# Optimization experiments

Hardware: AMD Instinct MI355X
Metric: run time of the kernel (lower is better)

The kernel has to match this reference:

```python
import jax, jax.numpy as jnp
import numpy as np

NUM_REGIONS = 32   # region labels are 1..NUM_REGIONS, 0 = background
EPS = 1e-8


def setup_inputs() -> dict:
    key = jax.random.key(0)
    k1, k2 = jax.random.split(key)
    B, D, H, W = 4, 160, 192, 192
    x = jax.random.normal(k1, (B, 1, D, H, W), dtype=jnp.float32)
    # precomputed connected-component label map (0 = background)
    region_map = jax.random.randint(k2, (B, D, H, W), 0, NUM_REGIONS + 1, dtype=jnp.int32)
    return {"x": x, "region_map": region_map}


def _per_volume_sums(xf, seg):
    # xf: [V] sigmoid probs, seg: [V] region ids in [0, NUM_REGIONS]
    xs = jax.ops.segment_sum(xf, seg, num_segments=NUM_REGIONS + 1)
    cnt = jax.ops.segment_sum(jnp.ones_like(xf), seg, num_segments=NUM_REGIONS + 1)
    return xs, cnt


def reference(x, region_map):
    B = x.shape[0]
    probs = jax.nn.sigmoid(x)                      # x.dim()==5 -> sigmoid
    xf = probs.reshape(B, -1)                      # [B, V]
    seg = region_map.reshape(B, -1)                # [B, V]
    xs, cnt = jax.vmap(_per_volume_sums)(xf, seg)  # [B, R+1] each
    xs_r = xs[:, 1:]                               # per-region sum of sigmoid(x)
    cnt_r = cnt[:, 1:]                             # per-region voxel count (= sum of binary y)
    # dice over the region: y==1 inside the region, so intersection == xs_r
    dice = 2.0 * xs_r / (xs_r + cnt_r + EPS)       # [B, R]
    valid = cnt_r > 0                              # region actually present
    n_valid = jnp.sum(valid, axis=-1)              # [B]
    mean_dice = jnp.sum(jnp.where(valid, dice, 0.0), axis=-1) / jnp.maximum(n_valid, 1)
    loss_b = jnp.where(n_valid > 0, 1.0 - mean_dice, 1.0)  # num_features==0 -> loss 1.0
    return jnp.mean(loss_b)
```

## Files before the change

kernel.cpp:

```cpp
#include <hip/hip_runtime.h>

#define NUM_REGIONS 32
#define NBINS 33
#define BATCH 4
#define DHW (160*192*192)
#define NVEC_PER_BATCH (DHW/4)
#define BLOCKS_PER_BATCH 512
#define NBLOCKS (BATCH*BLOCKS_PER_BATCH)
#define VEC_PER_BLOCK (NVEC_PER_BATCH/BLOCKS_PER_BATCH)
#define LDS_STRIDE 257
#define EPS 1e-8f

__global__ __launch_bounds__(256) void region_sums_kernel(
    const float* __restrict__ x,
    const int*   __restrict__ seg,
    float*       __restrict__ ws)
{
    __shared__ float hist[NBINS * LDS_STRIDE];
    const int tid = threadIdx.x;

    for (int i = tid; i < NBINS * LDS_STRIDE; i += 256) hist[i] = 0.0f;
    __syncthreads();

    const int  batch = blockIdx.x >> 9;
    const int  local = blockIdx.x & 511;
    const long vbase = (long)batch * NVEC_PER_BATCH + (long)local * VEC_PER_BLOCK;

    const float4* __restrict__ xv4 = (const float4*)x;
    const int4*   __restrict__ sv4 = (const int4*)seg;

    int    v  = tid;
    float4 xv = xv4[vbase + v];
    int4   sv = sv4[vbase + v];

    while (true) {
        int vn = v + 256;
        float4 xvn; int4 svn;
        bool more = (vn < VEC_PER_BLOCK);
        if (more) { xvn = xv4[vbase + vn]; svn = sv4[vbase + vn]; }

        float p0 = __fdividef(1.0f, 1.0f + __expf(-xv.x)) + 256.0f;
        float p1 = __fdividef(1.0f, 1.0f + __expf(-xv.y)) + 256.0f;
        float p2 = __fdividef(1.0f, 1.0f + __expf(-xv.z)) + 256.0f;
        float p3 = __fdividef(1.0f, 1.0f + __expf(-xv.w)) + 256.0f;

        hist[sv.x * LDS_STRIDE + tid] += p0;
        hist[sv.y * LDS_STRIDE + tid] += p1;
        hist[sv.z * LDS_STRIDE + tid] += p2;
        hist[sv.w * LDS_STRIDE + tid] += p3;

        if (!more) break;
        v = vn; xv = xvn; sv = svn;
    }
    __syncthreads();

    if (tid >= 1 && tid <= NUM_REGIONS) {
        float xs = 0.0f, cnt = 0.0f;
        #pragma unroll 8
        for (int t = 0; t < 256; ++t) {
            float V = hist[tid * LDS_STRIDE + t];
            float c = floorf(V * (1.0f / 256.0f));
            cnt += c;
            xs  += V - 256.0f * c;
        }
        atomicAdd(&ws[batch * NBINS + tid], xs);
        atomicAdd(&ws[BATCH * NBINS + batch * NBINS + tid], cnt);
    }
}

__global__ void region_dice_final_kernel(
    const float* __restrict__ ws,
    float*       __restrict__ out)
{
    const int lane = threadIdx.x;
    float loss_sum = 0.0f;

    for (int b = 0; b < BATCH; ++b) {
        bool  valid = false;
        float dice  = 0.0f;
        if (lane >= 1 && lane <= NUM_REGIONS) {
            float xs  = ws[b * NBINS + lane];
            float cnt = ws[BATCH * NBINS + b * NBINS + lane];
            valid = (cnt > 0.0f);
            if (valid) dice = 2.0f * xs / (xs + cnt + EPS);
        }
        unsigned long long m = __ballot(valid);
        int n_valid = __popcll(m);

        float s = dice;
        #pragma unroll
        for (int off = 32; off >= 1; off >>= 1) s += __shfl_down(s, off);

        float mean_dice = s / (float)((n_valid > 1) ? n_valid : 1);
        float loss_b    = (n_valid > 0) ? (1.0f - mean_dice) : 1.0f;
        loss_sum += loss_b;
    }

    if (lane == 0) out[0] = loss_sum * (1.0f / BATCH);
}

extern "C" void kernel_launch(void* const* d_in, const int* in_sizes, int n_in,
                              void* d_out, int out_size, void* d_ws, size_t ws_size,
                              hipStream_t stream)
{
    const float* x   = (const float*)d_in[0];
    const int*   seg = (const int*)d_in[1];
    float*       ws  = (float*)d_ws;

    hipMemsetAsync(d_ws, 0, 2 * BATCH * NBINS * sizeof(float), stream);

    region_sums_kernel<<<NBLOCKS, 256, 0, stream>>>(x, seg, ws);
    region_dice_final_kernel<<<1, 64, 0, stream>>>(ws, (float*)d_out);
}
```

Measured before the change: 223.6 us.

## Share histogram columns between thread pairs with LDS atomics and parallelize reduction

New measurement: 262.6 us. 17.4% more time.

```diff
diff --git a/kernel.cpp b/kernel.cpp
--- a/kernel.cpp
+++ b/kernel.cpp
@@ -5,10 +5,11 @@
 #define BATCH 4
 #define DHW (160*192*192)
 #define NVEC_PER_BATCH (DHW/4)
-#define BLOCKS_PER_BATCH 512
+#define BLOCKS_PER_BATCH 384
 #define NBLOCKS (BATCH*BLOCKS_PER_BATCH)
 #define VEC_PER_BLOCK (NVEC_PER_BATCH/BLOCKS_PER_BATCH)
-#define LDS_STRIDE 257
+#define ITERS (VEC_PER_BLOCK/256)
+#define COL_STRIDE 129
 #define EPS 1e-8f
 
 __global__ __launch_bounds__(256) void region_sums_kernel(
@@ -16,55 +17,71 @@
     const int*   __restrict__ seg,
     float*       __restrict__ ws)
 {
-    __shared__ float hist[NBINS * LDS_STRIDE];
+    __shared__ float hist[NBINS * COL_STRIDE];
+    __shared__ float part_xs [8][NBINS];
+    __shared__ float part_cnt[8][NBINS];
+
     const int tid = threadIdx.x;
+    const int col = tid >> 1;
 
-    for (int i = tid; i < NBINS * LDS_STRIDE; i += 256) hist[i] = 0.0f;
+    for (int i = tid; i < NBINS * COL_STRIDE; i += 256) hist[i] = 0.0f;
     __syncthreads();
 
-    const int  batch = blockIdx.x >> 9;
-    const int  local = blockIdx.x & 511;
-    const long vbase = (long)batch * NVEC_PER_BATCH + (long)local * VEC_PER_BLOCK;
+    const int batch = blockIdx.x / BLOCKS_PER_BATCH;
+    const int local = blockIdx.x - batch * BLOCKS_PER_BATCH;
+    const int vbase = batch * NVEC_PER_BATCH + local * VEC_PER_BLOCK + tid;
 
     const float4* __restrict__ xv4 = (const float4*)x;
     const int4*   __restrict__ sv4 = (const int4*)seg;
 
-    int    v  = tid;
-    float4 xv = xv4[vbase + v];
-    int4   sv = sv4[vbase + v];
+    float4 xA = xv4[vbase];       int4 sA = sv4[vbase];
+    float4 xB = xv4[vbase + 256]; int4 sB = sv4[vbase + 256];
 
-    while (true) {
-        int vn = v + 256;
-        float4 xvn; int4 svn;
-        bool more = (vn < VEC_PER_BLOCK);
-        if (more) { xvn = xv4[vbase + vn]; svn = sv4[vbase + vn]; }
+    for (int k = 0; k < ITERS; ++k) {
+        int kn = (k + 2 < ITERS) ? (k + 2) : (ITERS - 1);
+        float4 xN = xv4[vbase + kn * 256];
+        int4   sN = sv4[vbase + kn * 256];
 
-        float p0 = __fdividef(1.0f, 1.0f + __expf(-xv.x)) + 256.0f;
-        float p1 = __fdividef(1.0f, 1.0f + __expf(-xv.y)) + 256.0f;
-        float p2 = __fdividef(1.0f, 1.0f + __expf(-xv.z)) + 256.0f;
-        float p3 = __fdividef(1.0f, 1.0f + __expf(-xv.w)) + 256.0f;
+        float p0 = __fdividef(1.0f, 1.0f + __expf(-xA.x)) + 256.0f;
+        float p1 = __fdividef(1.0f, 1.0f + __expf(-xA.y)) + 256.0f;
+        float p2 = __fdividef(1.0f, 1.0f + __expf(-xA.z)) + 256.0f;
+        float p3 = __fdividef(1.0f, 1.0f + __expf(-xA.w)) + 256.0f;
 
-        hist[sv.x * LDS_STRIDE + tid] += p0;
-        hist[sv.y * LDS_STRIDE + tid] += p1;
-        hist[sv.z * LDS_STRIDE + tid] += p2;
-        hist[sv.w * LDS_STRIDE + tid] += p3;
+        atomicAdd(&hist[sA.x * COL_STRIDE + col], p0);
+        atomicAdd(&hist[sA.y * COL_STRIDE + col], p1);
+        atomicAdd(&hist[sA.z * COL_STRIDE + col], p2);
+        atomicAdd(&hist[sA.w * COL_STRIDE + col], p3);
 
-        if (!more) break;
-        v = vn; xv = xvn; sv = svn;
+        xA = xB; sA = sB; xB = xN; sB = sN;
     }
     __syncthreads();
 
-    if (tid >= 1 && tid <= NUM_REGIONS) {
+    {
+        const int bin = (tid & 31) + 1;
+        const int g   = tid >> 5;
         float xs = 0.0f, cnt = 0.0f;
-        #pragma unroll 8
-        for (int t = 0; t < 256; ++t) {
-            float V = hist[tid * LDS_STRIDE + t];
+        #pragma unroll
+        for (int j = 0; j < 16; ++j) {
+            float V = hist[bin * COL_STRIDE + g * 16 + j];
             float c = floorf(V * (1.0f / 256.0f));
             cnt += c;
             xs  += V - 256.0f * c;
         }
-        atomicAdd(&ws[batch * NBINS + tid], xs);
-        atomicAdd(&ws[BATCH * NBINS + batch * NBINS + tid], cnt);
+        part_xs [g][bin] = xs;
+        part_cnt[g][bin] = cnt;
+    }
+    __syncthreads();
+
+    if (tid < 32) {
+        const int bin = tid + 1;
+        float xs = 0.0f, cnt = 0.0f;
+        #pragma unroll
+        for (int g = 0; g < 8; ++g) {
+            xs  += part_xs [g][bin];
+            cnt += part_cnt[g][bin];
+        }
+        atomicAdd(&ws[batch * NBINS + bin], xs);
+        atomicAdd(&ws[BATCH * NBINS + batch * NBINS + bin], cnt);
     }
 }
 
```
